# Optimization experiments

Hardware: AMD Instinct MI355X
Metric: run time of the kernel (lower is better)

The kernel has to match this reference:

```python
import jax, jax.numpy as jnp
import numpy as np

# Production-scale 3D conv: B=4, C=64->64, 32^3 volume, 3x3x3 kernel, stride 1, pad 1.
B, CIN, COUT = 4, 64, 64
KSIZE = (3, 3, 3)
STRIDE = (1, 1, 1)
PAD = 1
SPATIAL = (32, 32, 32)


def setup_inputs() -> dict:
    key = jax.random.key(0)
    k1, k2, k3 = jax.random.split(key, 3)
    x = jax.random.normal(k1, (B, CIN) + SPATIAL, dtype=jnp.float32)
    weight = jax.random.normal(k2, (COUT, CIN) + KSIZE, dtype=jnp.float32)
    bias = jax.random.normal(k3, (COUT,), dtype=jnp.float32)
    return {"x": x, "weight": weight, "bias": bias}


def reference(x, weight, bias):
    # The original materializes all sliding-window patches via nested unfold and
    # contracts with einsum('bci...,oci->bo...'). That is exactly a standard
    # cross-correlation (torch-style conv). We express the same math as a direct
    # convolution, avoiding the O(kernel_volume) patch blowup.
    out = jax.lax.conv_general_dilated(
        x,
        weight,
        window_strides=STRIDE,
        padding=[(PAD, PAD)] * 3,
        dimension_numbers=("NCDHW", "OIDHW", "NCDHW"),
    )
    return out + bias.reshape(1, -1, 1, 1, 1)
```

## Files before the change

### kernel.cpp

```cpp
#include <hip/hip_runtime.h>
#include <hip/hip_bf16.h>

#define WS_W_OFF    0
#define WS_ZERO_OFF 221184
#define WS_XT_OFF   262144

typedef __attribute__((ext_vector_type(8))) short s16x8;
typedef __attribute__((ext_vector_type(4))) float f32x4;

#define GLOBAL_AS __attribute__((address_space(1)))
#define LDS_AS    __attribute__((address_space(3)))

__device__ __forceinline__ unsigned short f2bf(float f) {
  unsigned u = __builtin_bit_cast(unsigned, f);
  u = u + 0x7fffu + ((u >> 16) & 1u);
  return (unsigned short)(u >> 16);
}

__global__ void prep_kernel(const float* __restrict__ x,
                            const float* __restrict__ w,
                            unsigned short* __restrict__ wsw,
                            float* __restrict__ zeros,
                            unsigned short* __restrict__ xt) {
  int blk = blockIdx.x;
  if (blk < 432) {
    int t = blk * 256 + threadIdx.x;
    int tap  = t % 27;
    int cin  = (t / 27) & 63;
    int cout = t / (27 * 64);
    int h   = cin >> 5;
    int q   = (cin >> 3) & 3;
    int j   = cin & 7;
    int nf  = cout >> 4;
    int lane = q * 16 + (cout & 15);
    int dst = (((tap * 2 + h) * 4 + nf) * 64 + lane) * 8 + j;
    wsw[dst] = f2bf(w[t]);
    if (t < 64) zeros[t] = 0.0f;
  } else {
    int t  = (blk - 432) * 256 + threadIdx.x;
    int s  = t & 32767;
    int c8 = (t >> 15) & 7;
    int b  = t >> 18;
    const float* src = x + (size_t)(b * 64 + c8 * 8) * 32768 + s;
    s16x8 v;
    #pragma unroll
    for (int k = 0; k < 8; ++k) v[k] = (short)f2bf(src[(size_t)k * 32768]);
    *(s16x8*)(xt + (size_t)(b * 32768 + s) * 64 + c8 * 8) = v;
  }
}

__global__ __launch_bounds__(256, 2) void conv_kernel(const float* __restrict__ bias,
                                                      float* __restrict__ out,
                                                      const char* __restrict__ ws) {
  __shared__ unsigned char halo[52 * 1024];

  const int tid  = threadIdx.x;
  const int lane = tid & 63;
  const int w    = tid >> 6;
  const int logical = (blockIdx.x & 7) * 64 + (blockIdx.x >> 3);
  const int yt = logical & 7, zt = (logical >> 3) & 15, b = logical >> 7;
  const int z0 = zt * 2, y0 = yt * 4;
  const int zo  = w >> 1;
  const int yo2 = (w & 1) * 2;

  const int r15 = lane & 15;
  const int hi4 = lane >> 4;

  const int sl_sub   = lane >> 2;
  const int sl_chunk = lane & 3;

  auto stage = [&](int h) {
    for (int g = w; g < 52; g += 4) {
      int pos = g * 16 + sl_sub;
      int hz = pos / 204; int rem = pos - hz * 204;
      int hy = rem / 34;  int hx = rem - hy * 34;
      int gz = z0 + hz - 1, gy = y0 + hy - 1, gx = hx - 1;
      bool inb = (pos < 816) & ((unsigned)gz < 32u) &
                 ((unsigned)gy < 32u) & ((unsigned)gx < 32u);
      int s = (gz * 32 + gy) * 32 + gx;
      int src = inb ? (WS_XT_OFF + (b * 32768 + s) * 128 + h * 64 + sl_chunk * 16)
                    : WS_ZERO_OFF;
      __builtin_amdgcn_global_load_lds(
          (const GLOBAL_AS void*)(ws + src),
          (LDS_AS void*)(&halo[g * 1024 + lane * 16]),
          16, 0, 0);
    }
  };

  const s16x8* __restrict__ wfr = (const s16x8*)(ws + WS_W_OFF);

  f32x4 zero4 = {0.f, 0.f, 0.f, 0.f};
  f32x4 acc[4][4];
  #pragma unroll
  for (int mf = 0; mf < 4; ++mf)
    #pragma unroll
    for (int nf = 0; nf < 4; ++nf) acc[mf][nf] = zero4;

  s16x8 B0[4], B1[4], B2[4], A0[4], A1[4], A2[4];

  auto loadB = [&](s16x8* dst, int h, int tap) {
    #pragma unroll
    for (int nf = 0; nf < 4; ++nf)
      dst[nf] = wfr[((tap * 2 + h) * 4 + nf) * 64 + lane];
  };

  auto loadA = [&](s16x8* a, int tap) {
    int kd = tap / 9; int r9 = tap - kd * 9;
    int kh = r9 / 3;  int kw = r9 - kh * 3;
    int base = ((zo + kd) * 6 + (yo2 + kh)) * 34 + kw + r15;
    #pragma unroll
    for (int mf = 0; mf < 4; ++mf) {
      int pos = base + (mf >> 1) * 34 + (mf & 1) * 16;
      a[mf] = *(const s16x8*)&halo[pos * 64 + hi4 * 16];
    }
  };

  auto compute = [&](const s16x8* a, const s16x8* B) {
    #pragma unroll
    for (int mf = 0; mf < 4; ++mf)
      #pragma unroll
      for (int nf = 0; nf < 4; ++nf)
        acc[mf][nf] = __builtin_amdgcn_mfma_f32_16x16x32_bf16(
            a[mf], B[nf], acc[mf][nf], 0, 0, 0);
  };

  auto khalf = [&](int h) {
    loadA(A0, 0);
    #pragma unroll 1
    for (int t = 0; t < 8; ++t) {
      loadB(B2, h, 3 * t + 2); loadA(A1, 3 * t + 1); compute(A0, B0);
      loadB(B0, h, 3 * t + 3); loadA(A2, 3 * t + 2); compute(A1, B1);
      loadB(B1, h, 3 * t + 4); loadA(A0, 3 * t + 3); compute(A2, B2);
    }
    loadB(B2, h, 26); loadA(A1, 25); compute(A0, B0);
    loadA(A2, 26);    compute(A1, B1);
    compute(A2, B2);
  };

  stage(0);
  loadB(B0, 0, 0); loadB(B1, 0, 1);
  __syncthreads();
  khalf(0);

  loadB(B0, 1, 0); loadB(B1, 1, 1);
  __syncthreads();
  stage(1);
  __syncthreads();
  khalf(1);

  const int z = z0 + zo;
  #pragma unroll
  for (int nf = 0; nf < 4; ++nf) {
    int cout = nf * 16 + r15;
    float bv = bias[cout];
    #pragma unroll
    for (int mf = 0; mf < 4; ++mf) {
      int y  = y0 + yo2 + (mf >> 1);
      int x0 = (mf & 1) * 16 + 4 * hi4;
      float* orow = out + ((size_t)((b * 64 + cout) * 32 + z) * 32 + y) * 32;
      f32x4 v;
      #pragma unroll
      for (int r = 0; r < 4; ++r) v[r] = acc[mf][nf][r] + bv;
      *(f32x4*)&orow[x0] = v;
    }
  }
}

extern "C" void kernel_launch(void* const* d_in, const int* in_sizes, int n_in,
                              void* d_out, int out_size, void* d_ws, size_t ws_size,
                              hipStream_t stream) {
  const float* x    = (const float*)d_in[0];
  const float* wgt  = (const float*)d_in[1];
  const float* bias = (const float*)d_in[2];
  float* out = (float*)d_out;
  char* ws = (char*)d_ws;

  prep_kernel<<<4528, 256, 0, stream>>>(x, wgt,
                                        (unsigned short*)(ws + WS_W_OFF),
                                        (float*)(ws + WS_ZERO_OFF),
                                        (unsigned short*)(ws + WS_XT_OFF));
  conv_kernel<<<512, 256, 0, stream>>>(bias, out, ws);
}
```

Baseline: 46.20 us.

## Stage conv weight fragments through double-buffered LDS instead of per-wave global loads

Weight fragments for each tap are now copied once per block into a two-slot LDS buffer with global_load_lds, and each wave reads them from LDS. Previously all four waves loaded the same weights from global memory into triple-buffered registers. The change cuts redundant global/L2 weight traffic and lowers register use (fewer A/B fragment sets). In exchange it adds a block-wide barrier after every tap, which can serialize waves and expose latency, and it adds 8KB of LDS per block.

```diff
diff --git a/kernel.cpp b/kernel.cpp
--- a/kernel.cpp
+++ b/kernel.cpp
@@ -52,7 +52,8 @@
 __global__ __launch_bounds__(256, 2) void conv_kernel(const float* __restrict__ bias,
                                                       float* __restrict__ out,
                                                       const char* __restrict__ ws) {
-  __shared__ unsigned char halo[52 * 1024];
+  __shared__ __align__(16) unsigned char halo[52 * 1024];
+  __shared__ __align__(16) unsigned char blds[2][4096];
 
   const int tid  = threadIdx.x;
   const int lane = tid & 63;
@@ -69,7 +70,7 @@
   const int sl_sub   = lane >> 2;
   const int sl_chunk = lane & 3;
 
-  auto stage = [&](int h) {
+  auto stage_halo = [&](int h) {
     for (int g = w; g < 52; g += 4) {
       int pos = g * 16 + sl_sub;
       int hz = pos / 204; int rem = pos - hz * 204;
@@ -87,7 +88,12 @@
     }
   };
 
-  const s16x8* __restrict__ wfr = (const s16x8*)(ws + WS_W_OFF);
+  auto stage_B = [&](int h, int tap, int pbuf) {
+    __builtin_amdgcn_global_load_lds(
+        (const GLOBAL_AS void*)(ws + WS_W_OFF + (tap * 2 + h) * 4096 + tid * 16),
+        (LDS_AS void*)(&blds[pbuf][tid * 16]),
+        16, 0, 0);
+  };
 
   f32x4 zero4 = {0.f, 0.f, 0.f, 0.f};
   f32x4 acc[4][4];
@@ -96,12 +102,12 @@
     #pragma unroll
     for (int nf = 0; nf < 4; ++nf) acc[mf][nf] = zero4;
 
-  s16x8 B0[4], B1[4], B2[4], A0[4], A1[4], A2[4];
+  s16x8 Br[4], A0[4], A1[4];
 
-  auto loadB = [&](s16x8* dst, int h, int tap) {
+  auto loadBregs = [&](s16x8* dst, int pbuf) {
     #pragma unroll
     for (int nf = 0; nf < 4; ++nf)
-      dst[nf] = wfr[((tap * 2 + h) * 4 + nf) * 64 + lane];
+      dst[nf] = *(const s16x8*)&blds[pbuf][(nf * 64 + lane) * 16];
   };
 
   auto loadA = [&](s16x8* a, int tap) {
@@ -124,29 +130,30 @@
             a[mf], B[nf], acc[mf][nf], 0, 0, 0);
   };
 
-  auto khalf = [&](int h) {
+  #pragma unroll 1
+  for (int h = 0; h < 2; ++h) {
+    if (h) __syncthreads();
+    stage_halo(h);
+    stage_B(h, 0, 0);
+    __syncthreads();
+
     loadA(A0, 0);
     #pragma unroll 1
-    for (int t = 0; t < 8; ++t) {
-      loadB(B2, h, 3 * t + 2); loadA(A1, 3 * t + 1); compute(A0, B0);
-      loadB(B0, h, 3 * t + 3); loadA(A2, 3 * t + 2); compute(A1, B1);
-      loadB(B1, h, 3 * t + 4); loadA(A0, 3 * t + 3); compute(A2, B2);
+    for (int tt = 0; tt < 13; ++tt) {
+      loadBregs(Br, 0);
+      stage_B(h, 2 * tt + 1, 1);
+      loadA(A1, 2 * tt + 1);
+      compute(A0, Br);
+      __syncthreads();
+      loadBregs(Br, 1);
+      stage_B(h, 2 * tt + 2, 0);
+      loadA(A0, 2 * tt + 2);
+      compute(A1, Br);
+      __syncthreads();
     }
-    loadB(B2, h, 26); loadA(A1, 25); compute(A0, B0);
-    loadA(A2, 26);    compute(A1, B1);
-    compute(A2, B2);
-  };
-
-  stage(0);
-  loadB(B0, 0, 0); loadB(B1, 0, 1);
-  __syncthreads();
-  khalf(0);
-
-  loadB(B0, 1, 0); loadB(B1, 1, 1);
-  __syncthreads();
-  stage(1);
-  __syncthreads();
-  khalf(1);
+    loadBregs(Br, 0);
+    compute(A0, Br);
+  }
 
   const int z = z0 + zo;
   #pragma unroll
```

Result: slower. 48.22 us (+4.4%).

## Switch conv MFMA to 32x32x16 tiles with swizzled LDS halo and full unroll

Applied to the files above, without the earlier changes.

Replaces the 16x16x32 bf16 MFMA tiling with 32x32x16 MFMA tiles: four 16-float accumulators, weights re-laid out in prep to match the new B-fragment layout, and an adjusted output store mapping. The LDS halo is written and read with an XOR swizzle on the 16-byte chunk index to cut bank conflicts on A-fragment reads. The tap loop is fully unrolled with a three-slot register ring. The aim is fewer MFMA issues and LDS reads per output, at the cost of more code and register pressure.

```diff
diff --git a/kernel.cpp b/kernel.cpp
--- a/kernel.cpp
+++ b/kernel.cpp
@@ -5,8 +5,9 @@
 #define WS_ZERO_OFF 221184
 #define WS_XT_OFF   262144
 
-typedef __attribute__((ext_vector_type(8))) short s16x8;
-typedef __attribute__((ext_vector_type(4))) float f32x4;
+typedef __attribute__((ext_vector_type(8)))  short s16x8;
+typedef __attribute__((ext_vector_type(4)))  float f32x4;
+typedef __attribute__((ext_vector_type(16))) float f32x16;
 
 #define GLOBAL_AS __attribute__((address_space(1)))
 #define LDS_AS    __attribute__((address_space(3)))
@@ -28,12 +29,15 @@
     int tap  = t % 27;
     int cin  = (t / 27) & 63;
     int cout = t / (27 * 64);
-    int h   = cin >> 5;
-    int q   = (cin >> 3) & 3;
-    int j   = cin & 7;
-    int nf  = cout >> 4;
-    int lane = q * 16 + (cout & 15);
-    int dst = (((tap * 2 + h) * 4 + nf) * 64 + lane) * 8 + j;
+    int h  = cin >> 5;
+    int c5 = cin & 31;
+    int ks = c5 >> 4;
+    int hi = (c5 >> 3) & 1;
+    int j  = c5 & 7;
+    int nt = cout >> 5;
+    int l  = hi * 32 + (cout & 31);
+    int f  = nt * 2 + ks;
+    int dst = (((tap * 2 + h) * 4 + f) * 64 + l) * 8 + j;
     wsw[dst] = f2bf(w[t]);
     if (t < 64) zeros[t] = 0.0f;
   } else {
@@ -52,7 +56,7 @@
 __global__ __launch_bounds__(256, 2) void conv_kernel(const float* __restrict__ bias,
                                                       float* __restrict__ out,
                                                       const char* __restrict__ ws) {
-  __shared__ unsigned char halo[52 * 1024];
+  __shared__ __align__(16) unsigned char halo[52 * 1024];
 
   const int tid  = threadIdx.x;
   const int lane = tid & 63;
@@ -63,13 +67,13 @@
   const int zo  = w >> 1;
   const int yo2 = (w & 1) * 2;
 
-  const int r15 = lane & 15;
-  const int hi4 = lane >> 4;
+  const int q31 = lane & 31;
+  const int hi  = lane >> 5;
 
   const int sl_sub   = lane >> 2;
-  const int sl_chunk = lane & 3;
+  const int sl_chunk = (lane & 3) ^ ((lane >> 3) & 3);
 
-  auto stage = [&](int h) {
+  auto stage_halo = [&](int h) {
     for (int g = w; g < 52; g += 4) {
       int pos = g * 16 + sl_sub;
       int hz = pos / 204; int rem = pos - hz * 204;
@@ -89,79 +93,90 @@
 
   const s16x8* __restrict__ wfr = (const s16x8*)(ws + WS_W_OFF);
 
-  f32x4 zero4 = {0.f, 0.f, 0.f, 0.f};
-  f32x4 acc[4][4];
+  f32x16 acc[2][2];
   #pragma unroll
-  for (int mf = 0; mf < 4; ++mf)
+  for (int mt = 0; mt < 2; ++mt)
     #pragma unroll
-    for (int nf = 0; nf < 4; ++nf) acc[mf][nf] = zero4;
+    for (int nt = 0; nt < 2; ++nt)
+      #pragma unroll
+      for (int r = 0; r < 16; ++r) acc[mt][nt][r] = 0.0f;
 
-  s16x8 B0[4], B1[4], B2[4], A0[4], A1[4], A2[4];
+  s16x8 Ab[3][4], Bb[3][4];
+  const int pA0 = (zo * 6 + yo2) * 34 + q31;
+  const int pA1 = pA0 + 34;
 
-  auto loadB = [&](s16x8* dst, int h, int tap) {
+  auto loadB = [&](int slot, int h, int tap) {
     #pragma unroll
-    for (int nf = 0; nf < 4; ++nf)
-      dst[nf] = wfr[((tap * 2 + h) * 4 + nf) * 64 + lane];
+    for (int f = 0; f < 4; ++f)
+      Bb[slot][f] = wfr[((tap * 2 + h) * 4 + f) * 64 + lane];
   };
 
-  auto loadA = [&](s16x8* a, int tap) {
-    int kd = tap / 9; int r9 = tap - kd * 9;
-    int kh = r9 / 3;  int kw = r9 - kh * 3;
-    int base = ((zo + kd) * 6 + (yo2 + kh)) * 34 + kw + r15;
+  auto loadA = [&](int slot, int tap) {
+    const int kd = tap / 9, r9 = tap - kd * 9;
+    const int kh = r9 / 3, kw = r9 - kh * 3;
+    const int d  = (kd * 6 + kh) * 34 + kw;
     #pragma unroll
-    for (int mf = 0; mf < 4; ++mf) {
-      int pos = base + (mf >> 1) * 34 + (mf & 1) * 16;
-      a[mf] = *(const s16x8*)&halo[pos * 64 + hi4 * 16];
+    for (int mt = 0; mt < 2; ++mt) {
+      int p = (mt ? pA1 : pA0) + d;
+      #pragma unroll
+      for (int ks = 0; ks < 2; ++ks) {
+        int swz = ((ks << 1) | hi) ^ ((p >> 1) & 3);
+        Ab[slot][mt * 2 + ks] = *(const s16x8*)&halo[(p << 6) + (swz << 4)];
+      }
     }
   };
 
-  auto compute = [&](const s16x8* a, const s16x8* B) {
+  auto compute = [&](int slot) {
     #pragma unroll
-    for (int mf = 0; mf < 4; ++mf)
+    for (int ks = 0; ks < 2; ++ks)
       #pragma unroll
-      for (int nf = 0; nf < 4; ++nf)
-        acc[mf][nf] = __builtin_amdgcn_mfma_f32_16x16x32_bf16(
-            a[mf], B[nf], acc[mf][nf], 0, 0, 0);
+      for (int mt = 0; mt < 2; ++mt)
+        #pragma unroll
+        for (int nt = 0; nt < 2; ++nt)
+          acc[mt][nt] = __builtin_amdgcn_mfma_f32_32x32x16_bf16(
+              Ab[slot][mt * 2 + ks], Bb[slot][nt * 2 + ks], acc[mt][nt], 0, 0, 0);
   };
 
-  auto khalf = [&](int h) {
-    loadA(A0, 0);
-    #pragma unroll 1
-    for (int t = 0; t < 8; ++t) {
-      loadB(B2, h, 3 * t + 2); loadA(A1, 3 * t + 1); compute(A0, B0);
-      loadB(B0, h, 3 * t + 3); loadA(A2, 3 * t + 2); compute(A1, B1);
-      loadB(B1, h, 3 * t + 4); loadA(A0, 3 * t + 3); compute(A2, B2);
+  auto run27 = [&](int h) {
+    loadA(0, 0); loadA(1, 1);
+    #pragma unroll
+    for (int tap = 0; tap < 27; ++tap) {
+      if (tap < 25) {
+        loadB((tap + 2) % 3, h, tap + 2);
+        loadA((tap + 2) % 3, tap + 2);
+      }
+      compute(tap % 3);
     }
-    loadB(B2, h, 26); loadA(A1, 25); compute(A0, B0);
-    loadA(A2, 26);    compute(A1, B1);
-    compute(A2, B2);
   };
 
-  stage(0);
-  loadB(B0, 0, 0); loadB(B1, 0, 1);
+  stage_halo(0);
+  loadB(0, 0, 0); loadB(1, 0, 1);
   __syncthreads();
-  khalf(0);
+  run27(0);
 
-  loadB(B0, 1, 0); loadB(B1, 1, 1);
+  loadB(0, 1, 0); loadB(1, 1, 1);
   __syncthreads();
-  stage(1);
+  stage_halo(1);
   __syncthreads();
-  khalf(1);
+  run27(1);
 
   const int z = z0 + zo;
   #pragma unroll
-  for (int nf = 0; nf < 4; ++nf) {
-    int cout = nf * 16 + r15;
+  for (int nt = 0; nt < 2; ++nt) {
+    int cout = nt * 32 + q31;
     float bv = bias[cout];
     #pragma unroll
-    for (int mf = 0; mf < 4; ++mf) {
-      int y  = y0 + yo2 + (mf >> 1);
-      int x0 = (mf & 1) * 16 + 4 * hi4;
+    for (int mt = 0; mt < 2; ++mt) {
+      int y = y0 + yo2 + mt;
       float* orow = out + ((size_t)((b * 64 + cout) * 32 + z) * 32 + y) * 32;
-      f32x4 v;
       #pragma unroll
-      for (int r = 0; r < 4; ++r) v[r] = acc[mf][nf][r] + bv;
-      *(f32x4*)&orow[x0] = v;
+      for (int q = 0; q < 4; ++q) {
+        int x0 = q * 8 + hi * 4;
+        f32x4 v;
+        #pragma unroll
+        for (int r = 0; r < 4; ++r) v[r] = acc[mt][nt][q * 4 + r] + bv;
+        *(f32x4*)&orow[x0] = v;
+      }
     }
   }
 }
```

Measured after the change: 50.05 us. 8.3% more time.
